# Optimization experiments

Measured on AMD Instinct MI355X. Metric: run time of the kernel, lower is better.

The kernel has to match this reference:

```python
import jax, jax.numpy as jnp
import numpy as np

N_QUBITS = 4
N_LAYERS = 3
INV_SQRT2 = 0.7071067811865476
BSZ = 262144


def _apply_ry(state, wire, theta):
    # state: [B,2,2,2,2] complex; theta: [B] (per-batch rotation angle)
    s = jnp.moveaxis(state, wire + 1, -1)
    a0, a1 = s[..., 0], s[..., 1]
    c = jnp.cos(theta * 0.5)[:, None, None, None]
    sn = jnp.sin(theta * 0.5)[:, None, None, None]
    out = jnp.stack([c * a0 - sn * a1, sn * a0 + c * a1], axis=-1)
    return jnp.moveaxis(out, -1, wire + 1)


def _apply_h(state, wire):
    s = jnp.moveaxis(state, wire + 1, -1)
    a0, a1 = s[..., 0], s[..., 1]
    out = jnp.stack([(a0 + a1) * INV_SQRT2, (a0 - a1) * INV_SQRT2], axis=-1)
    return jnp.moveaxis(out, -1, wire + 1)


def _apply_crz(state, cw, tw, phi):
    # controlled-RZ: phase exp(-/+ i*phi/2) on |c=1,t=0/1>; phi is a scalar param
    s = jnp.moveaxis(state, (cw + 1, tw + 1), (-2, -1))
    phase = jnp.exp(1j * phi * jnp.array([-0.5, 0.5], dtype=jnp.float32)).astype(s.dtype)
    s = s.at[..., 1, :].multiply(phase)
    return jnp.moveaxis(s, (-2, -1), (cw + 1, tw + 1))


def _circuit(angles, weights):
    # angles: [B,4]; weights: [12]; returns PauliZ expvals [B,4]
    B = angles.shape[0]
    state = jnp.zeros((B, 2, 2, 2, 2), jnp.complex64).at[:, 0, 0, 0, 0].set(1.0)
    for i in range(N_QUBITS):
        state = _apply_ry(state, i, angles[:, i])
    for l in range(N_LAYERS):
        lp = weights[N_QUBITS * l: N_QUBITS * (l + 1)]
        for i in range(N_QUBITS):
            state = _apply_crz(state, i, (i + 1) % N_QUBITS, lp[i])
        for i in range(N_QUBITS):
            state = _apply_h(state, i)
    p = state.real ** 2 + state.imag ** 2  # [B,2,2,2,2] probabilities
    z = jnp.stack(
        [jnp.take(p, 0, axis=w + 1).sum(axis=(1, 2, 3))
         - jnp.take(p, 1, axis=w + 1).sum(axis=(1, 2, 3))
         for w in range(N_QUBITS)],
        axis=-1,
    )
    return z


def setup_inputs() -> dict:
    key = jax.random.key(0)
    k1, k2, k3, k4 = jax.random.split(key, 4)
    x = jax.random.uniform(k1, (BSZ, 16), dtype=jnp.float32)
    weights = jax.random.normal(k2, (N_LAYERS * N_QUBITS,), dtype=jnp.float32)
    lin_w = jax.random.normal(k3, (2, 16), dtype=jnp.float32) * 0.25
    lin_b = jax.random.normal(k4, (2,), dtype=jnp.float32) * 0.1
    return {"x": x, "weights": weights, "lin_w": lin_w, "lin_b": lin_b}


def reference(x, weights, lin_w, lin_b):
    bsz = x.shape[0]
    # 4x4 image -> four 2x2 patches in loop order (0,0),(0,2),(2,0),(2,2);
    # each patch flattened row-major: [x[j,k], x[j,k+1], x[j+1,k], x[j+1,k+1]]
    xv = x.reshape(bsz, 2, 2, 2, 2).transpose(0, 1, 3, 2, 4).reshape(bsz * 4, 4)
    q = _circuit(xv, weights).reshape(bsz, 16)  # patch-major feature order as in torch cat
    logits = q @ lin_w.T + lin_b
    return jax.nn.softmax(logits, axis=1)
```

## Files before the change

kernel.cpp:

```cpp
#include <hip/hip_runtime.h>


__device__ __forceinline__ float layer_angle(const float* __restrict__ w,
                                             int l, int idx) {
    float ang = 0.f;
    #pragma unroll
    for (int g = 0; g < 4; ++g) {
        int cb = (idx >> (3 - g)) & 1;
        int tb = (idx >> (3 - ((g + 1) & 3))) & 1;
        if (cb) ang += (tb ? 0.5f : -0.5f) * w[l * 4 + g];
    }
    return ang;
}

__global__ __launch_bounds__(1024) void fused_qcircuit(
    const float* __restrict__ x,
    const float* __restrict__ weights,
    const float* __restrict__ lin_w,
    const float* __restrict__ lin_b,
    float* __restrict__ out,
    int nrows)
{
    __shared__ float2 U1[256], U2[256], U[256];
    __shared__ float zeta[4][16];
    __shared__ float G[4][256];
    __shared__ float A[4][3][64];
    __shared__ float B[4][9][16];
    __shared__ float C1[4][27][4];
    __shared__ __align__(16) float tabs[4][9][12];

    int t = threadIdx.x;
    int i = t >> 4, j = t & 15;

    int b = blockIdx.x * blockDim.x + t;
    int bc = b < nrows ? b : 0;
    const float4* xp = (const float4*)(x + (size_t)bc * 16);
    float4 xa = xp[0], xb = xp[1], xc = xp[2], xd = xp[3];

    if (t < 256) {
        float sgn = (__popc(i & j) & 1) ? -1.f : 1.f;
        float a = layer_angle(weights, 0, j);
        U1[t] = make_float2(sgn * __cosf(a), sgn * __sinf(a));
    }
    if (t < 64) {
        int s = t >> 4, k = t & 15;
        float z = 0.f;
        #pragma unroll
        for (int w = 0; w < 4; ++w) {
            float sg = ((k >> (3 - w)) & 1) ? -1.f : 1.f;
            z += (lin_w[s * 4 + w] - lin_w[16 + s * 4 + w]) * sg;
        }
        zeta[s][k] = z;
    }
    __syncthreads();
    if (t < 256) {
        float ar = 0.f, ai = 0.f;
        for (int k = 0; k < 16; ++k) {
            float sgn = (__popc(i & k) & 1) ? -1.f : 1.f;
            float a = layer_angle(weights, 1, k);
            float cr = sgn * __cosf(a), ci = sgn * __sinf(a);
            float2 u = U1[k * 16 + j];
            ar += cr * u.x - ci * u.y;
            ai += cr * u.y + ci * u.x;
        }
        U2[t] = make_float2(ar, ai);
    }
    __syncthreads();
    if (t < 256) {
        float ar = 0.f, ai = 0.f;
        for (int k = 0; k < 16; ++k) {
            float sgn = (__popc(i & k) & 1) ? -1.f : 1.f;
            float a = layer_angle(weights, 2, k);
            float cr = sgn * __cosf(a), ci = sgn * __sinf(a);
            float2 u = U2[k * 16 + j];
            ar += cr * u.x - ci * u.y;
            ai += cr * u.y + ci * u.x;
        }
        U[t] = make_float2(ar, ai);
    }
    __syncthreads();
    if (t < 256) {
        float g[4] = {0, 0, 0, 0};
        for (int k = 0; k < 16; ++k) {
            float2 uki = U[k * 16 + i], ukj = U[k * 16 + j];
            float p = uki.x * ukj.x + uki.y * ukj.y;
            #pragma unroll
            for (int s = 0; s < 4; ++s) g[s] += zeta[s][k] * p;
        }
        #pragma unroll
        for (int s = 0; s < 4; ++s) G[s][t] = g[s];
    }
    __syncthreads();
    for (int e = t; e < 768; e += 1024) {
        int m = e / 192, r = e % 192;
        int t3 = r / 64, q = r % 64;
        int ih = q >> 3, jh = q & 7;
        float g00 = G[m][(ih * 2 + 0) * 16 + jh * 2 + 0];
        float g01 = G[m][(ih * 2 + 0) * 16 + jh * 2 + 1];
        float g10 = G[m][(ih * 2 + 1) * 16 + jh * 2 + 0];
        float g11 = G[m][(ih * 2 + 1) * 16 + jh * 2 + 1];
        A[m][t3][q] = (t3 == 0) ? g00 + g11 : (t3 == 1) ? g00 - g11 : g01 + g10;
    }
    __syncthreads();
    for (int e = t; e < 576; e += 1024) {
        int m = e / 144, r = e % 144;
        int t2 = r / 48; r %= 48;
        int t3 = r / 16, q = r % 16;
        int ih = q >> 2, jh = q & 3;
        float a00 = A[m][t3][(ih * 2 + 0) * 8 + jh * 2 + 0];
        float a01 = A[m][t3][(ih * 2 + 0) * 8 + jh * 2 + 1];
        float a10 = A[m][t3][(ih * 2 + 1) * 8 + jh * 2 + 0];
        float a11 = A[m][t3][(ih * 2 + 1) * 8 + jh * 2 + 1];
        B[m][t2 * 3 + t3][q] = (t2 == 0) ? a00 + a11
                             : (t2 == 1) ? a00 - a11 : a01 + a10;
    }
    __syncthreads();
    for (int e = t; e < 432; e += 1024) {
        int m = e / 108, r = e % 108;
        int t1 = r / 36; r %= 36;
        int t23 = r / 4, q = r % 4;
        int ih = q >> 1, jh = q & 1;
        float b00 = B[m][t23][(ih * 2 + 0) * 4 + jh * 2 + 0];
        float b01 = B[m][t23][(ih * 2 + 0) * 4 + jh * 2 + 1];
        float b10 = B[m][t23][(ih * 2 + 1) * 4 + jh * 2 + 0];
        float b11 = B[m][t23][(ih * 2 + 1) * 4 + jh * 2 + 1];
        C1[m][t1 * 9 + t23][q] = (t1 == 0) ? b00 + b11
                               : (t1 == 1) ? b00 - b11 : b01 + b10;
    }
    __syncthreads();
    {
        const float scale = 1.f / 65536.f;
        float bias = lin_b[0] - lin_b[1];
        for (int e = t; e < 324; e += 1024) {
            int m = e / 81, r = e % 81;
            int t0 = r / 27, t123 = r % 27;
            const float* c = C1[m][t123];
            float v = (t0 == 0) ? c[0] + c[3] : (t0 == 1) ? c[0] - c[3]
                                              : c[1] + c[2];
            float val = v * scale;
            if (e == 0) val += bias;
            int t1 = t123 / 9, k = t123 % 9;
            tabs[m][t0 * 3 + t1][k] = val;
        }
    }
    __syncthreads();

    float xs[16] = {xa.x, xa.y, xa.z, xa.w, xb.x, xb.y, xb.z, xb.w,
                    xc.x, xc.y, xc.z, xc.w, xd.x, xd.y, xd.z, xd.w};
    float d = 0.f;
    #pragma unroll
    for (int s = 0; s < 4; ++s) {
        const int b0 = ((s >> 1) << 3) + ((s & 1) << 1);
        float C0, S0, C1v, S1, C2, S2, C3, S3;
        __sincosf(xs[b0],     &S0,  &C0);
        __sincosf(xs[b0 + 1], &S1,  &C1v);
        __sincosf(xs[b0 + 4], &S2,  &C2);
        __sincosf(xs[b0 + 5], &S3,  &C3);
        #pragma unroll
        for (int t0 = 0; t0 < 3; ++t0) {
            float acc = 0.f;
            #pragma unroll
            for (int t1 = 0; t1 < 3; ++t1) {
                const float* tp = &tabs[s][t0 * 3 + t1][0];
                float4 q0 = *(const float4*)tp;
                float4 q1 = *(const float4*)(tp + 4);
                float  k8 = tp[8];
                float u0 = fmaf(S3, q0.z, fmaf(C3, q0.y, q0.x));
                float u1 = fmaf(S3, q1.y, fmaf(C3, q1.x, q0.w));
                float u2 = fmaf(S3, k8,   fmaf(C3, q1.w, q1.z));
                float a1 = fmaf(S2, u2, fmaf(C2, u1, u0));
                acc = (t1 == 0) ? acc + a1
                    : (t1 == 1) ? fmaf(C1v, a1, acc)
                                : fmaf(S1,  a1, acc);
            }
            d = (t0 == 0) ? d + acc
              : (t0 == 1) ? fmaf(C0, acc, d)
                          : fmaf(S0, acc, d);
        }
    }

    if (b < nrows) {
        float p0 = 1.f / (1.f + __expf(-d));
        *(float2*)(out + (size_t)b * 2) = make_float2(p0, 1.f - p0);
    }

    for (int row = b + gridDim.x * blockDim.x; row < nrows;
         row += gridDim.x * blockDim.x) {
        const float4* xq = (const float4*)(x + (size_t)row * 16);
        float4 ya = xq[0], yb = xq[1], yc = xq[2], yd = xq[3];
        float ys[16] = {ya.x, ya.y, ya.z, ya.w, yb.x, yb.y, yb.z, yb.w,
                        yc.x, yc.y, yc.z, yc.w, yd.x, yd.y, yd.z, yd.w};
        float dd = 0.f;
        #pragma unroll
        for (int s = 0; s < 4; ++s) {
            const int b0 = ((s >> 1) << 3) + ((s & 1) << 1);
            float C0, S0, C1v, S1, C2, S2, C3, S3;
            __sincosf(ys[b0],     &S0,  &C0);
            __sincosf(ys[b0 + 1], &S1,  &C1v);
            __sincosf(ys[b0 + 4], &S2,  &C2);
            __sincosf(ys[b0 + 5], &S3,  &C3);
            #pragma unroll
            for (int t0 = 0; t0 < 3; ++t0) {
                float acc = 0.f;
                #pragma unroll
                for (int t1 = 0; t1 < 3; ++t1) {
                    const float* tp = &tabs[s][t0 * 3 + t1][0];
                    float4 q0 = *(const float4*)tp;
                    float4 q1 = *(const float4*)(tp + 4);
                    float  k8 = tp[8];
                    float u0 = fmaf(S3, q0.z, fmaf(C3, q0.y, q0.x));
                    float u1 = fmaf(S3, q1.y, fmaf(C3, q1.x, q0.w));
                    float u2 = fmaf(S3, k8,   fmaf(C3, q1.w, q1.z));
                    float a1 = fmaf(S2, u2, fmaf(C2, u1, u0));
                    acc = (t1 == 0) ? acc + a1
                        : (t1 == 1) ? fmaf(C1v, a1, acc)
                                    : fmaf(S1,  a1, acc);
                }
                dd = (t0 == 0) ? dd + acc
                   : (t0 == 1) ? fmaf(C0, acc, dd)
                               : fmaf(S0, acc, dd);
            }
        }
        float p0 = 1.f / (1.f + __expf(-dd));
        *(float2*)(out + (size_t)row * 2) = make_float2(p0, 1.f - p0);
    }
}

extern "C" void kernel_launch(void* const* d_in, const int* in_sizes, int n_in,
                              void* d_out, int out_size, void* d_ws, size_t ws_size,
                              hipStream_t stream) {
    const float* x       = (const float*)d_in[0];
    const float* weights = (const float*)d_in[1];
    const float* lin_w   = (const float*)d_in[2];
    const float* lin_b   = (const float*)d_in[3];
    float* out = (float*)d_out;

    int nrows = in_sizes[0] / 16;
    int block = 1024;
    int grid = (nrows + block - 1) / block;
    if (grid < 1) grid = 1;
    fused_qcircuit<<<grid, block, 0, stream>>>(x, weights, lin_w, lin_b, out, nrows);
}
```

Baseline: 73.78 us.

## Split each row across two threads with shuffle reduction and smaller blocks

Each row's four patch contributions are now split between two adjacent threads (two patches each), combined with a lane shuffle, and each thread writes one output probability. Blocks shrink to 512 threads covering 256 rows, so the grid has four times as many blocks, and the input load moves after the table build. The aim is more parallelism and less per-thread register pressure. In exchange, every block repeats the table precomputation, and that prologue now runs four times as often in total.

```diff
diff --git a/kernel.cpp b/kernel.cpp
--- a/kernel.cpp
+++ b/kernel.cpp
@@ -13,7 +13,7 @@
     return ang;
 }
 
-__global__ __launch_bounds__(1024) void fused_qcircuit(
+__global__ __launch_bounds__(512, 8) void fused_qcircuit(
     const float* __restrict__ x,
     const float* __restrict__ weights,
     const float* __restrict__ lin_w,
@@ -32,11 +32,6 @@
     int t = threadIdx.x;
     int i = t >> 4, j = t & 15;
 
-    int b = blockIdx.x * blockDim.x + t;
-    int bc = b < nrows ? b : 0;
-    const float4* xp = (const float4*)(x + (size_t)bc * 16);
-    float4 xa = xp[0], xb = xp[1], xc = xp[2], xd = xp[3];
-
     if (t < 256) {
         float sgn = (__popc(i & j) & 1) ? -1.f : 1.f;
         float a = layer_angle(weights, 0, j);
@@ -91,7 +86,7 @@
         for (int s = 0; s < 4; ++s) G[s][t] = g[s];
     }
     __syncthreads();
-    for (int e = t; e < 768; e += 1024) {
+    for (int e = t; e < 768; e += 512) {
         int m = e / 192, r = e % 192;
         int t3 = r / 64, q = r % 64;
         int ih = q >> 3, jh = q & 7;
@@ -102,7 +97,7 @@
         A[m][t3][q] = (t3 == 0) ? g00 + g11 : (t3 == 1) ? g00 - g11 : g01 + g10;
     }
     __syncthreads();
-    for (int e = t; e < 576; e += 1024) {
+    for (int e = t; e < 576; e += 512) {
         int m = e / 144, r = e % 144;
         int t2 = r / 48; r %= 48;
         int t3 = r / 16, q = r % 16;
@@ -115,7 +110,7 @@
                              : (t2 == 1) ? a00 - a11 : a01 + a10;
     }
     __syncthreads();
-    for (int e = t; e < 432; e += 1024) {
+    for (int e = t; e < 432; e += 512) {
         int m = e / 108, r = e % 108;
         int t1 = r / 36; r %= 36;
         int t23 = r / 4, q = r % 4;
@@ -128,10 +123,17 @@
                                : (t1 == 1) ? b00 - b11 : b01 + b10;
     }
     __syncthreads();
+
+    const int h = t & 1;
+    int row = blockIdx.x * 256 + (t >> 1);
+    int rc = row < nrows ? row : 0;
+    const float4* xp = (const float4*)(x + (size_t)rc * 16);
+    float4 va = xp[2 * h], vb = xp[2 * h + 1];
+
     {
         const float scale = 1.f / 65536.f;
         float bias = lin_b[0] - lin_b[1];
-        for (int e = t; e < 324; e += 1024) {
+        for (int e = t; e < 324; e += 512) {
             int m = e / 81, r = e % 81;
             int t0 = r / 27, t123 = r % 27;
             const float* c = C1[m][t123];
@@ -145,33 +147,33 @@
     }
     __syncthreads();
 
-    float xs[16] = {xa.x, xa.y, xa.z, xa.w, xb.x, xb.y, xb.z, xb.w,
-                    xc.x, xc.y, xc.z, xc.w, xd.x, xd.y, xd.z, xd.w};
     float d = 0.f;
     #pragma unroll
-    for (int s = 0; s < 4; ++s) {
-        const int b0 = ((s >> 1) << 3) + ((s & 1) << 1);
+    for (int k = 0; k < 2; ++k) {
+        const int si = h * 2 + k;
+        float a0 = k ? va.z : va.x, a1 = k ? va.w : va.y;
+        float a2 = k ? vb.z : vb.x, a3 = k ? vb.w : vb.y;
         float C0, S0, C1v, S1, C2, S2, C3, S3;
-        __sincosf(xs[b0],     &S0,  &C0);
-        __sincosf(xs[b0 + 1], &S1,  &C1v);
-        __sincosf(xs[b0 + 4], &S2,  &C2);
-        __sincosf(xs[b0 + 5], &S3,  &C3);
+        __sincosf(a0, &S0, &C0);
+        __sincosf(a1, &S1, &C1v);
+        __sincosf(a2, &S2, &C2);
+        __sincosf(a3, &S3, &C3);
         #pragma unroll
         for (int t0 = 0; t0 < 3; ++t0) {
             float acc = 0.f;
             #pragma unroll
             for (int t1 = 0; t1 < 3; ++t1) {
-                const float* tp = &tabs[s][t0 * 3 + t1][0];
+                const float* tp = &tabs[si][t0 * 3 + t1][0];
                 float4 q0 = *(const float4*)tp;
                 float4 q1 = *(const float4*)(tp + 4);
                 float  k8 = tp[8];
                 float u0 = fmaf(S3, q0.z, fmaf(C3, q0.y, q0.x));
                 float u1 = fmaf(S3, q1.y, fmaf(C3, q1.x, q0.w));
                 float u2 = fmaf(S3, k8,   fmaf(C3, q1.w, q1.z));
-                float a1 = fmaf(S2, u2, fmaf(C2, u1, u0));
-                acc = (t1 == 0) ? acc + a1
-                    : (t1 == 1) ? fmaf(C1v, a1, acc)
-                                : fmaf(S1,  a1, acc);
+                float a1v = fmaf(S2, u2, fmaf(C2, u1, u0));
+                acc = (t1 == 0) ? acc + a1v
+                    : (t1 == 1) ? fmaf(C1v, a1v, acc)
+                                : fmaf(S1,  a1v, acc);
             }
             d = (t0 == 0) ? d + acc
               : (t0 == 1) ? fmaf(C0, acc, d)
@@ -179,50 +181,51 @@
         }
     }
 
-    if (b < nrows) {
-        float p0 = 1.f / (1.f + __expf(-d));
-        *(float2*)(out + (size_t)b * 2) = make_float2(p0, 1.f - p0);
-    }
-
-    for (int row = b + gridDim.x * blockDim.x; row < nrows;
-         row += gridDim.x * blockDim.x) {
+    d += __shfl_xor(d, 1);
+    if (row < nrows) {
+        float p = 1.f / (1.f + __expf(h ? d : -d));
+        out[(size_t)row * 2 + h] = p;
+    }
+
+    for (row += gridDim.x * 256; row < nrows; row += gridDim.x * 256) {
         const float4* xq = (const float4*)(x + (size_t)row * 16);
-        float4 ya = xq[0], yb = xq[1], yc = xq[2], yd = xq[3];
-        float ys[16] = {ya.x, ya.y, ya.z, ya.w, yb.x, yb.y, yb.z, yb.w,
-                        yc.x, yc.y, yc.z, yc.w, yd.x, yd.y, yd.z, yd.w};
+        float4 wa = xq[2 * h], wb = xq[2 * h + 1];
         float dd = 0.f;
         #pragma unroll
-        for (int s = 0; s < 4; ++s) {
-            const int b0 = ((s >> 1) << 3) + ((s & 1) << 1);
+        for (int k = 0; k < 2; ++k) {
+            const int si = h * 2 + k;
+            float a0 = k ? wa.z : wa.x, a1 = k ? wa.w : wa.y;
+            float a2 = k ? wb.z : wb.x, a3 = k ? wb.w : wb.y;
             float C0, S0, C1v, S1, C2, S2, C3, S3;
-            __sincosf(ys[b0],     &S0,  &C0);
-            __sincosf(ys[b0 + 1], &S1,  &C1v);
-            __sincosf(ys[b0 + 4], &S2,  &C2);
-            __sincosf(ys[b0 + 5], &S3,  &C3);
+            __sincosf(a0, &S0, &C0);
+            __sincosf(a1, &S1, &C1v);
+            __sincosf(a2, &S2, &C2);
+            __sincosf(a3, &S3, &C3);
             #pragma unroll
             for (int t0 = 0; t0 < 3; ++t0) {
                 float acc = 0.f;
                 #pragma unroll
                 for (int t1 = 0; t1 < 3; ++t1) {
-                    const float* tp = &tabs[s][t0 * 3 + t1][0];
+                    const float* tp = &tabs[si][t0 * 3 + t1][0];
                     float4 q0 = *(const float4*)tp;
                     float4 q1 = *(const float4*)(tp + 4);
                     float  k8 = tp[8];
                     float u0 = fmaf(S3, q0.z, fmaf(C3, q0.y, q0.x));
                     float u1 = fmaf(S3, q1.y, fmaf(C3, q1.x, q0.w));
                     float u2 = fmaf(S3, k8,   fmaf(C3, q1.w, q1.z));
-                    float a1 = fmaf(S2, u2, fmaf(C2, u1, u0));
-                    acc = (t1 == 0) ? acc + a1
-                        : (t1 == 1) ? fmaf(C1v, a1, acc)
-                                    : fmaf(S1,  a1, acc);
+                    float a1v = fmaf(S2, u2, fmaf(C2, u1, u0));
+                    acc = (t1 == 0) ? acc + a1v
+                        : (t1 == 1) ? fmaf(C1v, a1v, acc)
+                                    : fmaf(S1,  a1v, acc);
                 }
                 dd = (t0 == 0) ? dd + acc
                    : (t0 == 1) ? fmaf(C0, acc, dd)
                                : fmaf(S0, acc, dd);
             }
         }
-        float p0 = 1.f / (1.f + __expf(-dd));
-        *(float2*)(out + (size_t)row * 2) = make_float2(p0, 1.f - p0);
+        dd += __shfl_xor(dd, 1);
+        float p = 1.f / (1.f + __expf(h ? dd : -dd));
+        out[(size_t)row * 2 + h] = p;
     }
 }
 
@@ -236,8 +239,7 @@
     float* out = (float*)d_out;
 
     int nrows = in_sizes[0] / 16;
-    int block = 1024;
-    int grid = (nrows + block - 1) / block;
+    int grid = (nrows + 255) / 256;
     if (grid < 1) grid = 1;
-    fused_qcircuit<<<grid, block, 0, stream>>>(x, weights, lin_w, lin_b, out, nrows);
+    fused_qcircuit<<<grid, 512, 0, stream>>>(x, weights, lin_w, lin_b, out, nrows);
 }
```

After: 138.2 us. +87.3%, slower.
